# Optimization experiments

Hardware: AMD Instinct MI355X
Metric: run time of the kernel (lower is better)

## Reference

```python
import jax, jax.numpy as jnp
import numpy as np

N = 64
EPS = 1e-8


def setup_inputs() -> dict:
    key = jax.random.key(0)
    k1, k2, k3 = jax.random.split(key, 3)
    x = jax.random.normal(k1, (524288, N), dtype=jnp.float32)
    L = jax.random.uniform(k2, (2 * N, 2 * N), dtype=jnp.float32)
    R = jax.random.uniform(k3, (N, N), dtype=jnp.float32)
    return {"x": x, "L": L, "R": R}


def reference(x, L, R):
    n = N
    xr = x.reshape(n, -1)                      # (n, T)
    M = L @ L.T + EPS * jnp.eye(2 * n, dtype=L.dtype)
    M11 = M[:n, :n]
    M21 = M[:n, n:]   # note: original code names M[:n, n:] as M21
    M22 = M[n:, n:]
    A = 2.0 * (M11 + M22 + R - R.T)            # (n, n)
    A = jnp.linalg.inv(A) @ M21                # Koopman operator (n, n)
    return (A @ xr).reshape(-1, n)
```

## Files before the change

### kernel.cpp

```cpp
#include <hip/hip_runtime.h>

#define SN 524288

__global__ __launch_bounds__(256) void k_buildC(const float* __restrict__ L,
                                                const float* __restrict__ R,
                                                float* __restrict__ Ct) {
  __shared__ float4 Ls[4096];
  const float4* L4 = (const float4*)L;
  #pragma unroll
  for (int it = 0; it < 16; ++it) {
    int idx = threadIdx.x + it * 256;
    int row = idx >> 5, t4 = idx & 31;
    Ls[(row << 5) + (t4 ^ (row & 7))] = L4[idx];
  }
  __syncthreads();
  int g = blockIdx.x * 256 + threadIdx.x;
  int c = g >> 6;
  int i = g & 63;
  if (c < 64) {
    float d1 = 0.f, d2 = 0.f;
    #pragma unroll
    for (int t4 = 0; t4 < 32; ++t4) {
      float4 a1 = Ls[(i << 5) + (t4 ^ (i & 7))];
      float4 b1 = Ls[(c << 5) + (t4 ^ (c & 7))];
      float4 a2 = Ls[((64 + i) << 5) + (t4 ^ (i & 7))];
      float4 b2 = Ls[((64 + c) << 5) + (t4 ^ (c & 7))];
      d1 += a1.x * b1.x + a1.y * b1.y + a1.z * b1.z + a1.w * b1.w;
      d2 += a2.x * b2.x + a2.y * b2.y + a2.z * b2.z + a2.w * b2.w;
    }
    float val = 2.0f * (d1 + d2 + R[i * 64 + c] - R[c * 64 + i]);
    if (i == c) val += 4e-8f;
    Ct[c * 64 + i] = val;
  } else {
    int jj = c - 64;
    float d = 0.f;
    #pragma unroll
    for (int t4 = 0; t4 < 32; ++t4) {
      float4 a = Ls[(i << 5) + (t4 ^ (i & 7))];
      float4 b = Ls[((64 + jj) << 5) + (t4 ^ (jj & 7))];
      d += a.x * b.x + a.y * b.y + a.z * b.z + a.w * b.w;
    }
    Ct[c * 64 + i] = d;
  }
}

__global__ __launch_bounds__(256) void k_solve(const float* __restrict__ Ct,
                                               float* __restrict__ At) {
  __shared__ float colbuf[2][64];
  __shared__ __align__(16) float rowbuf[2][128];
  const int r = threadIdx.x & 63;
  const int cgrp = threadIdx.x >> 6;
  float creg[32];
  #pragma unroll
  for (int cc = 0; cc < 32; ++cc)
    creg[cc] = Ct[(cgrp * 32 + cc) * 64 + r];
  #pragma unroll
  for (int p = 0; p < 64; ++p) {
    const int pb = p & 1, pc = p >> 5, pi = p & 31;
    if (cgrp == pc) colbuf[pb][r] = creg[pi];
    if (r == p) {
      #pragma unroll
      for (int cc = 0; cc < 32; ++cc) rowbuf[pb][cgrp * 32 + cc] = creg[cc];
    }
    __syncthreads();
    const float f = colbuf[pb][r];
    const float inv = 1.0f / colbuf[pb][p];
    if (r == p) {
      #pragma unroll
      for (int cc = 0; cc < 32; ++cc) creg[cc] *= inv;
    } else {
      const float gg = f * inv;
      #pragma unroll
      for (int c4 = 0; c4 < 8; ++c4) {
        const float4 pv = *(const float4*)&rowbuf[pb][cgrp * 32 + c4 * 4];
        creg[c4 * 4 + 0] -= gg * pv.x;
        creg[c4 * 4 + 1] -= gg * pv.y;
        creg[c4 * 4 + 2] -= gg * pv.z;
        creg[c4 * 4 + 3] -= gg * pv.w;
      }
    }
  }
  if (cgrp >= 2) {
    #pragma unroll
    for (int cc = 0; cc < 32; ++cc) {
      int k = (cgrp - 2) * 32 + cc;
      At[k * 64 + r] = creg[cc];
    }
  }
}

__global__ __launch_bounds__(256) void k_apply(const float* __restrict__ x,
                                               const float* __restrict__ At,
                                               float* __restrict__ out) {
  __shared__ float4 Al[1024];
  const float4* At4 = (const float4*)At;
  #pragma unroll
  for (int it = 0; it < 4; ++it)
    Al[threadIdx.x + it * 256] = At4[threadIdx.x + it * 256];
  __syncthreads();
  const int j = blockIdx.x * 256 + threadIdx.x;
  float acc[64];
  #pragma unroll
  for (int i = 0; i < 64; ++i) acc[i] = 0.f;
  const float* xp = x + j;
  #pragma unroll 4
  for (int k = 0; k < 64; ++k) {
    const float xv = xp[k * SN];
    #pragma unroll
    for (int i4 = 0; i4 < 16; ++i4) {
      const float4 a = Al[(k << 4) + i4];
      acc[i4 * 4 + 0] += a.x * xv;
      acc[i4 * 4 + 1] += a.y * xv;
      acc[i4 * 4 + 2] += a.z * xv;
      acc[i4 * 4 + 3] += a.w * xv;
    }
  }
  float* op = out + j;
  #pragma unroll
  for (int i = 0; i < 64; ++i) op[i * SN] = acc[i];
}

extern "C" void kernel_launch(void* const* d_in, const int* in_sizes, int n_in,
                              void* d_out, int out_size, void* d_ws, size_t ws_size,
                              hipStream_t stream) {
  const float* x = (const float*)d_in[0];
  const float* L = (const float*)d_in[1];
  const float* R = (const float*)d_in[2];
  float* out = (float*)d_out;
  float* Ct = (float*)d_ws;
  float* At = Ct + 128 * 64;
  k_buildC<<<32, 256, 0, stream>>>(L, R, Ct);
  k_solve<<<1, 256, 0, stream>>>(Ct, At);
  k_apply<<<2048, 256, 0, stream>>>(x, At, out);
}
```

Measured before the change: 126.1 us.

## Retile apply kernel: split output rows across waves, vectorize columns, prefetch x

The apply kernel now gives each wave 16 of the 64 output rows and each lane 8 columns, loaded as two float4 vectors. Previously every thread computed all 64 rows for a single column. This lowers per-thread accumulator pressure, enables 128-bit loads and nontemporal 128-bit stores, and prefetches the next k-row of x while the current one is being computed. Each x element is now read by four waves, so more traffic goes through the L2 cache, and the grid is halved to 1024 blocks with a minimum-occupancy hint in the launch bounds.

```diff
diff --git a/kernel.cpp b/kernel.cpp
--- a/kernel.cpp
+++ b/kernel.cpp
@@ -1,6 +1,8 @@
 #include <hip/hip_runtime.h>
 
 #define SN 524288
+
+typedef float f32x4 __attribute__((ext_vector_type(4)));
 
 __global__ __launch_bounds__(256) void k_buildC(const float* __restrict__ L,
                                                 const float* __restrict__ R,
@@ -89,35 +91,67 @@
   }
 }
 
-__global__ __launch_bounds__(256) void k_apply(const float* __restrict__ x,
-                                               const float* __restrict__ At,
-                                               float* __restrict__ out) {
-  __shared__ float4 Al[1024];
-  const float4* At4 = (const float4*)At;
+__global__ __launch_bounds__(256, 3) void k_apply(const float* __restrict__ x,
+                                                  const float* __restrict__ At,
+                                                  float* __restrict__ out) {
+  __shared__ f32x4 Al[1024];
+  const f32x4* At4 = (const f32x4*)At;
   #pragma unroll
   for (int it = 0; it < 4; ++it)
     Al[threadIdx.x + it * 256] = At4[threadIdx.x + it * 256];
   __syncthreads();
-  const int j = blockIdx.x * 256 + threadIdx.x;
-  float acc[64];
+
+  const int lane = threadIdx.x & 63;
+  const int w = threadIdx.x >> 6;
+  const int c0 = blockIdx.x * 128 + lane;
+  const int c1 = c0 + 64;
+  const f32x4* x4 = (const f32x4*)x;
+  f32x4* out4 = (f32x4*)out;
+
+  float acc[16][8];
   #pragma unroll
-  for (int i = 0; i < 64; ++i) acc[i] = 0.f;
-  const float* xp = x + j;
-  #pragma unroll 4
+  for (int i = 0; i < 16; ++i)
+    #pragma unroll
+    for (int j = 0; j < 8; ++j) acc[i][j] = 0.f;
+
+  f32x4 xa = x4[c0];
+  f32x4 xb = x4[c1];
+  #pragma unroll 2
   for (int k = 0; k < 64; ++k) {
-    const float xv = xp[k * SN];
+    f32x4 na, nb;
+    if (k < 63) {
+      na = x4[(k + 1) * (SN / 4) + c0];
+      nb = x4[(k + 1) * (SN / 4) + c1];
+    }
     #pragma unroll
-    for (int i4 = 0; i4 < 16; ++i4) {
-      const float4 a = Al[(k << 4) + i4];
-      acc[i4 * 4 + 0] += a.x * xv;
-      acc[i4 * 4 + 1] += a.y * xv;
-      acc[i4 * 4 + 2] += a.z * xv;
-      acc[i4 * 4 + 3] += a.w * xv;
+    for (int q = 0; q < 4; ++q) {
+      const f32x4 a = Al[(k << 4) + (w << 2) + q];
+      #pragma unroll
+      for (int r = 0; r < 4; ++r) {
+        const float av = a[r];
+        const int il = q * 4 + r;
+        acc[il][0] += av * xa[0];
+        acc[il][1] += av * xa[1];
+        acc[il][2] += av * xa[2];
+        acc[il][3] += av * xa[3];
+        acc[il][4] += av * xb[0];
+        acc[il][5] += av * xb[1];
+        acc[il][6] += av * xb[2];
+        acc[il][7] += av * xb[3];
+      }
     }
+    xa = na;
+    xb = nb;
   }
-  float* op = out + j;
+
   #pragma unroll
-  for (int i = 0; i < 64; ++i) op[i * SN] = acc[i];
+  for (int il = 0; il < 16; ++il) {
+    const int i = w * 16 + il;
+    f32x4 v0 = {acc[il][0], acc[il][1], acc[il][2], acc[il][3]};
+    f32x4 v1 = {acc[il][4], acc[il][5], acc[il][6], acc[il][7]};
+    __builtin_nontemporal_store(v0, &out4[i * (SN / 4) + c0]);
+    __builtin_nontemporal_store(v1, &out4[i * (SN / 4) + c1]);
+  }
 }
 
 extern "C" void kernel_launch(void* const* d_in, const int* in_sizes, int n_in,
@@ -131,5 +165,5 @@
   float* At = Ct + 128 * 64;
   k_buildC<<<32, 256, 0, stream>>>(L, R, Ct);
   k_solve<<<1, 256, 0, stream>>>(Ct, At);
-  k_apply<<<2048, 256, 0, stream>>>(x, At, out);
+  k_apply<<<1024, 256, 0, stream>>>(x, At, out);
 }
```

Result: slower. 139.8 us (+10.9%).

## Fuse Gram build and solve into one block; split apply outputs per wave

Applied to the files above, without the earlier changes.

Merges the Gram-matrix build and the Gauss-Jordan solve into one single-block kernel, keeping the intermediate matrix in shared memory. This removes a launch and a global round trip, but all of the build work now runs on one CU. The apply kernel gives each wave half of the 64 outputs. It reads the operator through wave-uniform (scalar) global loads instead of LDS, and prefetches x four rows ahead. This cuts per-thread accumulator registers, but each x column is now read by two waves.

```diff
diff --git a/kernel.cpp b/kernel.cpp
--- a/kernel.cpp
+++ b/kernel.cpp
@@ -2,10 +2,16 @@
 
 #define SN 524288
 
-__global__ __launch_bounds__(256) void k_buildC(const float* __restrict__ L,
-                                                const float* __restrict__ R,
-                                                float* __restrict__ Ct) {
+typedef float f32x4 __attribute__((ext_vector_type(4)));
+
+__global__ __launch_bounds__(256) void k_prep(const float* __restrict__ L,
+                                              const float* __restrict__ R,
+                                              float* __restrict__ AtW) {
   __shared__ float4 Ls[4096];
+  __shared__ float Ct[128 * 64];
+  __shared__ float colbuf[2][64];
+  __shared__ __align__(16) float rowbuf[2][128];
+
   const float4* L4 = (const float4*)L;
   #pragma unroll
   for (int it = 0; it < 16; ++it) {
@@ -14,40 +20,40 @@
     Ls[(row << 5) + (t4 ^ (row & 7))] = L4[idx];
   }
   __syncthreads();
-  int g = blockIdx.x * 256 + threadIdx.x;
-  int c = g >> 6;
-  int i = g & 63;
-  if (c < 64) {
-    float d1 = 0.f, d2 = 0.f;
-    #pragma unroll
-    for (int t4 = 0; t4 < 32; ++t4) {
-      float4 a1 = Ls[(i << 5) + (t4 ^ (i & 7))];
-      float4 b1 = Ls[(c << 5) + (t4 ^ (c & 7))];
-      float4 a2 = Ls[((64 + i) << 5) + (t4 ^ (i & 7))];
-      float4 b2 = Ls[((64 + c) << 5) + (t4 ^ (c & 7))];
-      d1 += a1.x * b1.x + a1.y * b1.y + a1.z * b1.z + a1.w * b1.w;
-      d2 += a2.x * b2.x + a2.y * b2.y + a2.z * b2.z + a2.w * b2.w;
+
+  #pragma unroll
+  for (int it = 0; it < 32; ++it) {
+    int g = it * 256 + threadIdx.x;
+    int c = g >> 6;
+    int i = g & 63;
+    if (c < 64) {
+      float d1 = 0.f, d2 = 0.f;
+      #pragma unroll
+      for (int t4 = 0; t4 < 32; ++t4) {
+        float4 a1 = Ls[(i << 5) + (t4 ^ (i & 7))];
+        float4 b1 = Ls[(c << 5) + (t4 ^ (c & 7))];
+        float4 a2 = Ls[((64 + i) << 5) + (t4 ^ (i & 7))];
+        float4 b2 = Ls[((64 + c) << 5) + (t4 ^ (c & 7))];
+        d1 += a1.x * b1.x + a1.y * b1.y + a1.z * b1.z + a1.w * b1.w;
+        d2 += a2.x * b2.x + a2.y * b2.y + a2.z * b2.z + a2.w * b2.w;
+      }
+      float val = 2.0f * (d1 + d2 + R[i * 64 + c] - R[c * 64 + i]);
+      if (i == c) val += 4e-8f;
+      Ct[c * 64 + i] = val;
+    } else {
+      int jj = c - 64;
+      float d = 0.f;
+      #pragma unroll
+      for (int t4 = 0; t4 < 32; ++t4) {
+        float4 a = Ls[(i << 5) + (t4 ^ (i & 7))];
+        float4 b = Ls[((64 + jj) << 5) + (t4 ^ (jj & 7))];
+        d += a.x * b.x + a.y * b.y + a.z * b.z + a.w * b.w;
+      }
+      Ct[c * 64 + i] = d;
     }
-    float val = 2.0f * (d1 + d2 + R[i * 64 + c] - R[c * 64 + i]);
-    if (i == c) val += 4e-8f;
-    Ct[c * 64 + i] = val;
-  } else {
-    int jj = c - 64;
-    float d = 0.f;
-    #pragma unroll
-    for (int t4 = 0; t4 < 32; ++t4) {
-      float4 a = Ls[(i << 5) + (t4 ^ (i & 7))];
-      float4 b = Ls[((64 + jj) << 5) + (t4 ^ (jj & 7))];
-      d += a.x * b.x + a.y * b.y + a.z * b.z + a.w * b.w;
-    }
-    Ct[c * 64 + i] = d;
   }
-}
+  __syncthreads();
 
-__global__ __launch_bounds__(256) void k_solve(const float* __restrict__ Ct,
-                                               float* __restrict__ At) {
-  __shared__ float colbuf[2][64];
-  __shared__ __align__(16) float rowbuf[2][128];
   const int r = threadIdx.x & 63;
   const int cgrp = threadIdx.x >> 6;
   float creg[32];
@@ -84,40 +90,45 @@
     #pragma unroll
     for (int cc = 0; cc < 32; ++cc) {
       int k = (cgrp - 2) * 32 + cc;
-      At[k * 64 + r] = creg[cc];
+      AtW[((r >> 5) * 64 + k) * 32 + (r & 31)] = creg[cc];
     }
   }
 }
 
 __global__ __launch_bounds__(256) void k_apply(const float* __restrict__ x,
-                                               const float* __restrict__ At,
+                                               const float* __restrict__ AtW,
                                                float* __restrict__ out) {
-  __shared__ float4 Al[1024];
-  const float4* At4 = (const float4*)At;
+  const int lane = threadIdx.x & 63;
+  const int wv = threadIdx.x >> 6;
+  const int jw = wv & 1;
+  const int h = __builtin_amdgcn_readfirstlane(wv >> 1);
+  const int c = blockIdx.x * 128 + jw * 64 + lane;
+  const float* __restrict__ Ab = AtW + h * 64 * 32;
+
+  float acc[32];
   #pragma unroll
-  for (int it = 0; it < 4; ++it)
-    Al[threadIdx.x + it * 256] = At4[threadIdx.x + it * 256];
-  __syncthreads();
-  const int j = blockIdx.x * 256 + threadIdx.x;
-  float acc[64];
+  for (int i = 0; i < 32; ++i) acc[i] = 0.f;
+
+  const float* xc = x + c;
+  float xb[4];
   #pragma unroll
-  for (int i = 0; i < 64; ++i) acc[i] = 0.f;
-  const float* xp = x + j;
+  for (int d = 0; d < 4; ++d) xb[d] = xc[d * SN];
+
   #pragma unroll 4
   for (int k = 0; k < 64; ++k) {
-    const float xv = xp[k * SN];
+    const float xv = xb[k & 3];
+    const int kp = (k + 4 < 64) ? (k + 4) : 63;
+    xb[k & 3] = xc[kp * SN];
+    const float* __restrict__ ak = Ab + k * 32;
     #pragma unroll
-    for (int i4 = 0; i4 < 16; ++i4) {
-      const float4 a = Al[(k << 4) + i4];
-      acc[i4 * 4 + 0] += a.x * xv;
-      acc[i4 * 4 + 1] += a.y * xv;
-      acc[i4 * 4 + 2] += a.z * xv;
-      acc[i4 * 4 + 3] += a.w * xv;
-    }
+    for (int i = 0; i < 32; ++i)
+      acc[i] = fmaf(ak[i], xv, acc[i]);
   }
-  float* op = out + j;
+
+  float* oc = out + (h * 32) * SN + c;
   #pragma unroll
-  for (int i = 0; i < 64; ++i) op[i * SN] = acc[i];
+  for (int i = 0; i < 32; ++i)
+    oc[i * SN] = acc[i];
 }
 
 extern "C" void kernel_launch(void* const* d_in, const int* in_sizes, int n_in,
@@ -127,9 +138,7 @@
   const float* L = (const float*)d_in[1];
   const float* R = (const float*)d_in[2];
   float* out = (float*)d_out;
-  float* Ct = (float*)d_ws;
-  float* At = Ct + 128 * 64;
-  k_buildC<<<32, 256, 0, stream>>>(L, R, Ct);
-  k_solve<<<1, 256, 0, stream>>>(Ct, At);
-  k_apply<<<2048, 256, 0, stream>>>(x, At, out);
+  float* AtW = (float*)d_ws;
+  k_prep<<<1, 256, 0, stream>>>(L, R, AtW);
+  k_apply<<<4096, 256, 0, stream>>>(x, AtW, out);
 }
```

After: 162.1 us. 28.6% more time.
